# Performance work log

Measured on AMD Instinct MI355X. Metric: run time of the kernel, lower is better.

Reference implementation:

```python
import jax, jax.numpy as jnp
import numpy as np

B, N, K = 8, 4096, 5


def setup_inputs() -> dict:
    key = jax.random.key(0)
    ks = jax.random.split(key, 24)
    s = 0.05
    inp = {
        'pointcloud': jax.random.normal(ks[0], (B, 3, N, 1), jnp.float32),
        # local 1x1 conv stack (bias-free) + BN affine params (eval mode, stats=identity)
        'conv_w1': jax.random.normal(ks[1], (64, 3), jnp.float32) * s,
        'bn1_g': jnp.ones((64,), jnp.float32), 'bn1_b': jnp.zeros((64,), jnp.float32),
        'conv_w2': jax.random.normal(ks[2], (64, 64), jnp.float32) * s,
        'bn2_g': jnp.ones((64,), jnp.float32), 'bn2_b': jnp.zeros((64,), jnp.float32),
        'conv_w3': jax.random.normal(ks[3], (64, 64), jnp.float32) * s,
        'bn3_g': jnp.ones((64,), jnp.float32), 'bn3_b': jnp.zeros((64,), jnp.float32),
        'conv_w4': jax.random.normal(ks[4], (128, 64), jnp.float32) * s,
        'bn4_g': jnp.ones((128,), jnp.float32), 'bn4_b': jnp.zeros((128,), jnp.float32),
        # GCN layers
        'gc1_w': jax.random.normal(ks[5], (128, 128), jnp.float32) * s,
        'gc1_b': jnp.zeros((128,), jnp.float32),
        'gc2_w': jax.random.normal(ks[6], (128, 128), jnp.float32) * s,
        'gc2_b': jnp.zeros((128,), jnp.float32),
        'gc3_w': jax.random.normal(ks[7], (128, 256), jnp.float32) * s,
        'gc3_b': jnp.zeros((256,), jnp.float32),
        # MLP head
        'fc1_w': jax.random.normal(ks[8], (512, 256), jnp.float32) * s,
        'bnf1_g': jnp.ones((512,), jnp.float32), 'bnf1_b': jnp.zeros((512,), jnp.float32),
        'fc2_w': jax.random.normal(ks[9], (256, 512), jnp.float32) * s,
        'bnf2_g': jnp.ones((256,), jnp.float32), 'bnf2_b': jnp.zeros((256,), jnp.float32),
        'fc3_w': jax.random.normal(ks[10], (128, 256), jnp.float32) * s,
        'fc3_b': jnp.zeros((128,), jnp.float32),
    }
    return inp


def _cbr(h, w, g, b):
    # 1x1 conv (per-point linear) + BatchNorm(eval, identity stats) + ReLU
    return jax.nn.relu((h @ w.T) * g + b)


def reference(pointcloud, conv_w1, bn1_g, bn1_b, conv_w2, bn2_g, bn2_b,
              conv_w3, bn3_g, bn3_b, conv_w4, bn4_g, bn4_b,
              gc1_w, gc1_b, gc2_w, gc2_b, gc3_w, gc3_b,
              fc1_w, bnf1_g, bnf1_b, fc2_w, bnf2_g, bnf2_b, fc3_w, fc3_b):
    pts = pointcloud[..., 0]                       # [B,3,N]
    b, _, n = pts.shape

    # ---- LocalOperation: sort points by distance to centroid, gather ----
    centroid = pts.mean(axis=2, keepdims=True)     # [B,3,1]
    d_cent = ((pts - centroid) ** 2).sum(axis=1)   # [B,N]
    order = jnp.argsort(d_cent, axis=-1)           # [B,N]
    x = jnp.take_along_axis(pts, order[:, None, :], axis=2)  # [B,3,N]

    h = x.transpose(0, 2, 1)                       # [B,N,3]
    h = _cbr(h, conv_w1, bn1_g, bn1_b)             # [B,N,64]
    h = _cbr(h, conv_w2, bn2_g, bn2_b)
    h = _cbr(h, conv_w3, bn3_g, bn3_b)
    h = _cbr(h, conv_w4, bn4_g, bn4_b)             # [B,N,128]
    feat = h.reshape(b * n, 128)                   # node features

    # ---- KNN graph (k=5, within each cloud, self included like KDTree) ----
    sq = (pts ** 2).sum(axis=1)                                        # [B,N]
    d2 = sq[:, :, None] + sq[:, None, :] - 2.0 * jnp.einsum('bcn,bcm->bnm', pts, pts)
    _, nbr = jax.lax.top_k(-d2, K)                                     # [B,N,K]
    offsets = (jnp.arange(b) * n)[:, None, None]
    src = (nbr + offsets).reshape(-1)                                  # [B*N*K]
    dst = jnp.broadcast_to(jnp.arange(b * n).reshape(b, n, 1), (b, n, K)).reshape(-1)

    num_nodes = b * n
    ones = jnp.ones_like(src, jnp.float32)
    deg_out = jax.ops.segment_sum(ones, src, num_segments=num_nodes)
    deg_in = jax.ops.segment_sum(ones, dst, num_segments=num_nodes)
    norm_out = jax.lax.rsqrt(jnp.maximum(deg_out, 1.0))
    norm_in = jax.lax.rsqrt(jnp.maximum(deg_in, 1.0))

    def gcn(hh, w, bias):
        hw = (hh @ w) * norm_out[:, None]          # [BN,F] pre-normed features
        msg = hw[src]                              # gather
        agg = jax.ops.segment_sum(msg, dst, num_segments=num_nodes)  # scatter-add
        return agg * norm_in[:, None] + bias

    g = jax.nn.relu(gcn(feat, gc1_w, gc1_b))       # [BN,128]
    g = jax.nn.relu(gcn(g, gc2_w, gc2_b))          # [BN,128]
    g = gcn(g, gc3_w, gc3_b)                       # [BN,256]

    # ---- head (BN eval, dropout eval = identity) ----
    z = jax.nn.relu((g @ fc1_w.T) * bnf1_g + bnf1_b)   # [BN,512]
    z = jax.nn.relu((z @ fc2_w.T) * bnf2_g + bnf2_b)   # [BN,256]
    pooled = z.max(axis=0)                             # [256] global max over nodes
    out = pooled @ fc3_w.T + fc3_b                     # [128]
    return out
```

## Files before the change

kernel.cpp:

```cpp
#include <hip/hip_runtime.h>
#include <math.h>
#include <float.h>

#define NB 8
#define NP 4096
#define BN_ (NB*NP)
#define KNN 5
#define JCH 512
#define NJC (NP/JCH)

typedef unsigned short u16;
typedef __attribute__((ext_vector_type(8))) __bf16 bf16x8;
typedef __attribute__((ext_vector_type(4))) float f32x4;

__device__ __forceinline__ u16 f2bf(float x){
  unsigned u = __float_as_uint(x);
  u += 0x7fff + ((u>>16)&1);
  return (u16)(u>>16);
}
__device__ __forceinline__ float bf2f(u16 h){ return __uint_as_float(((unsigned)h)<<16); }


__global__ void k_centroid(const float* __restrict__ pc, float* __restrict__ dcent) {
  int b = blockIdx.x, tid = threadIdx.x;
  const float* px = pc + (size_t)b*3*NP;
  const float* py = px + NP;
  const float* pz = py + NP;
  double sx=0, sy=0, sz=0;
  for (int n = tid; n < NP; n += 256) { sx += px[n]; sy += py[n]; sz += pz[n]; }
  __shared__ double rx[256], ry[256], rz[256];
  rx[tid]=sx; ry[tid]=sy; rz[tid]=sz;
  __syncthreads();
  for (int s = 128; s > 0; s >>= 1) {
    if (tid < s) { rx[tid]+=rx[tid+s]; ry[tid]+=ry[tid+s]; rz[tid]+=rz[tid+s]; }
    __syncthreads();
  }
  __shared__ float cxs, cys, czs;
  if (tid == 0) {
    cxs = (float)(rx[0]/NP); cys = (float)(ry[0]/NP); czs = (float)(rz[0]/NP);
  }
  __syncthreads();
  float cx = cxs, cy = cys, cz = czs;
  for (int n = tid; n < NP; n += 256) {
    float dx = __fsub_rn(px[n], cx);
    float dy = __fsub_rn(py[n], cy);
    float dz = __fsub_rn(pz[n], cz);
    float d = __fadd_rn(__fadd_rn(__fmul_rn(dx,dx), __fmul_rn(dy,dy)), __fmul_rn(dz,dz));
    dcent[b*NP + n] = d;
  }
}

__global__ void __launch_bounds__(256) k_rank_part(const float* __restrict__ dcent,
                                                   int* __restrict__ rank) {
  int jc = blockIdx.x, ic = blockIdx.y, b = blockIdx.z;
  __shared__ float d[JCH];
  int j0 = jc*JCH;
  for (int n = threadIdx.x; n < JCH; n += 256) d[n] = dcent[b*NP + j0 + n];
  __syncthreads();
  int i = ic*256 + threadIdx.x;
  float di = dcent[b*NP + i];
  int cnt = 0;
  #pragma unroll 8
  for (int n = 0; n < JCH; ++n) {
    float dj = d[n];
    cnt += (dj < di) || (dj == di && (j0 + n) < i);
  }
  atomicAdd(&rank[b*NP + i], cnt);
}

__global__ void k_scatter(const int* __restrict__ rank, int* __restrict__ ord) {
  int idx = blockIdx.x*256 + threadIdx.x;
  int b = idx >> 12, i = idx & (NP-1);
  ord[b*NP + rank[idx]] = i;
}

__global__ void k_prep(const float* __restrict__ pc, const int* __restrict__ ord,
                       const float* __restrict__ dcent,
                       float4* __restrict__ srt, float* __restrict__ rc) {
  int idx = blockIdx.x*256 + threadIdx.x;
  int b = idx >> 12;
  int oi = ord[idx];
  const float* base = pc + (size_t)b*3*NP;
  float x = base[oi], y = base[NP+oi], z = base[2*NP+oi];
  float sq = __fadd_rn(__fadd_rn(__fmul_rn(x,x), __fmul_rn(y,y)), __fmul_rn(z,z));
  float4 v; v.x=x; v.y=y; v.z=z; v.w=sq;
  srt[idx] = v;
  rc[idx] = sqrtf(dcent[b*NP + oi]);
}

#define INS(dist, q) \
  if (dist < b4) { \
    if (dist < b3) { b4=b3; r4=r3; \
      if (dist < b2) { b3=b2; r3=r2; \
        if (dist < b1) { b2=b1; r2=r1; \
          if (dist < b0) { b1=b0; r1=r0; b0=dist; r0=(q); } \
          else { b1=dist; r1=(q); } \
        } else { b2=dist; r2=(q); } \
      } else { b3=dist; r3=(q); } \
    } else { b4=dist; r4=(q); } \
  }

__global__ void __launch_bounds__(256) k_knn_ann3(const float4* __restrict__ srt,
                                                  const float* __restrict__ rc,
                                                  const int* __restrict__ ord,
                                                  int* __restrict__ nbr,
                                                  int* __restrict__ deg) {
  __shared__ float4 tile[NP];
  __shared__ float rtile[NP];
  int b = blockIdx.x >> 7;
  int blk = blockIdx.x & 127;
  int gbase = b*NP;
  for (int t = threadIdx.x; t < NP; t += 256) {
    tile[t] = srt[gbase + t];
    rtile[t] = rc[gbase + t];
  }
  __syncthreads();

  const int lane = threadIdx.x & 63;
  const int wv   = threadIdx.x >> 6;
  const int grp  = lane >> 3;
  const int sub  = lane & 7;
  const int s_i  = blk*32 + wv*8 + grp;

  float4 p = tile[s_i];
  float xi=p.x, yi=p.y, zi=p.z, sqi=p.w;
  float ri = rtile[s_i];

  const bool is_hi = (sub < 4);
  int j = is_hi ? (s_i + sub) : (s_i - 1 - (sub - 4));
  const int step = is_hi ? 4 : -4;

  float b0=FLT_MAX, b1=FLT_MAX, b2=FLT_MAX, b3=FLT_MAX, b4=FLT_MAX;
  int r0=0, r1=0, r2=0, r3=0, r4=0;
  bool alive = ((unsigned)j < NP);

  while (__ballot(alive)) {
    int q[8]; float4 jp[8];
    #pragma unroll
    for (int t = 0; t < 8; ++t) {
      int qq = j + step*t;
      int qc = qq < 0 ? 0 : (qq > NP-1 ? NP-1 : qq);
      q[t] = qq;
      jp[t] = tile[qc];
    }
    #pragma unroll
    for (int t = 0; t < 8; ++t) {
      float dot = __fadd_rn(__fadd_rn(__fmul_rn(xi,jp[t].x), __fmul_rn(yi,jp[t].y)), __fmul_rn(zi,jp[t].z));
      float dist = __fsub_rn(__fadd_rn(sqi, jp[t].w), __fmul_rn(2.0f, dot));
      bool valid = alive && ((unsigned)q[t] < NP);
      if (!valid) dist = FLT_MAX;
      if (dist < b4) { INS(dist, q[t]) }
    }
    float bm = b4;
    bm = fminf(bm, __shfl_xor(bm, 1));
    bm = fminf(bm, __shfl_xor(bm, 2));
    bm = fminf(bm, __shfl_xor(bm, 4));
    float T = bm*1.0002f + 1e-9f;
    int qe = j + step*7;
    int qec = qe < 0 ? 0 : (qe > NP-1 ? NP-1 : qe);
    float dr = fabsf(ri - rtile[qec]);
    j += step*8;
    alive = alive && ((unsigned)j < NP) && (__fmul_rn(dr,dr) < T);
  }

  #pragma unroll
  for (int m = 1; m <= 4; m <<= 1) {
    float c0=__shfl_xor(b0,m), c1=__shfl_xor(b1,m), c2=__shfl_xor(b2,m),
          c3=__shfl_xor(b3,m), c4=__shfl_xor(b4,m);
    int   s0=__shfl_xor(r0,m), s1=__shfl_xor(r1,m), s2=__shfl_xor(r2,m),
          s3=__shfl_xor(r3,m), s4=__shfl_xor(r4,m);
    if (c0 < b4) { INS(c0, s0)
      if (c1 < b4) { INS(c1, s1)
        if (c2 < b4) { INS(c2, s2)
          if (c3 < b4) { INS(c3, s3)
            if (c4 < b4) { INS(c4, s4) }
          }
        }
      }
    }
  }

  if (sub == 0) {
    int oi = ord[gbase + s_i];
    int node = gbase + oi;
    int nb = node*KNN;
    int o0 = gbase + ord[gbase+r0], o1 = gbase + ord[gbase+r1], o2 = gbase + ord[gbase+r2];
    int o3 = gbase + ord[gbase+r3], o4 = gbase + ord[gbase+r4];
    nbr[nb+0]=o0; nbr[nb+1]=o1; nbr[nb+2]=o2; nbr[nb+3]=o3; nbr[nb+4]=o4;
    atomicAdd(&deg[o0],1); atomicAdd(&deg[o1],1); atomicAdd(&deg[o2],1);
    atomicAdd(&deg[o3],1); atomicAdd(&deg[o4],1);
  }
}

__global__ void k_norm(const int* __restrict__ deg, float* __restrict__ normo) {
  int i = blockIdx.x*256 + threadIdx.x;
  int d = deg[i]; if (d < 1) d = 1;
  normo[i] = 1.0f / sqrtf((float)d);
}

__global__ void k_cvt_all(const float* __restrict__ w2, const float* __restrict__ w3,
                          const float* __restrict__ w4, const float* __restrict__ gc1,
                          const float* __restrict__ gc2, const float* __restrict__ gc3,
                          const float* __restrict__ fc1, const float* __restrict__ fc2,
                          u16* o2, u16* o3, u16* o4, u16* og1, u16* og2, u16* og3,
                          u16* of1, u16* of2) {
  int i = blockIdx.x*256 + threadIdx.x;
  if (i < 4096) { o2[i] = f2bf(w2[i]); return; } i -= 4096;
  if (i < 4096) { o3[i] = f2bf(w3[i]); return; } i -= 4096;
  if (i < 8192) { o4[i] = f2bf(w4[i]); return; } i -= 8192;
  if (i < 16384) { int n=i>>7, k=i&127; og1[i] = f2bf(gc1[k*128+n]); return; } i -= 16384;
  if (i < 16384) { int n=i>>7, k=i&127; og2[i] = f2bf(gc2[k*128+n]); return; } i -= 16384;
  if (i < 32768) { int n=i>>7, k=i&127; og3[i] = f2bf(gc3[k*256+n]); return; } i -= 32768;
  if (i < 131072) { of1[i] = f2bf(fc1[i]); return; } i -= 131072;
  if (i < 131072) { of2[i] = f2bf(fc2[i]); }
}

__global__ void k_conv1(const float* __restrict__ pc, const int* __restrict__ ord,
                        const float* __restrict__ w, const float* __restrict__ g,
                        const float* __restrict__ bias, u16* __restrict__ outp) {
  int node = blockIdx.x*4 + (threadIdx.x >> 6);
  int o = threadIdx.x & 63;
  int b = node >> 12;
  int j = ord[node];
  const float* base = pc + (size_t)b*3*NP;
  float x = base[j], y = base[NP + j], z = base[2*NP + j];
  float acc = x*w[o*3+0] + y*w[o*3+1] + z*w[o*3+2];
  float v = fmaxf(acc*g[o] + bias[o], 0.0f);
  outp[(size_t)node*64 + o] = f2bf(v);
}

template<int BNT>
__global__ __launch_bounds__(256) void gemm_bf16(
    const u16* __restrict__ A, const u16* __restrict__ W,
    const float* __restrict__ gamma, const float* __restrict__ beta,
    const float* __restrict__ rowscale, void* __restrict__ Cout,
    int K, int Nc, int mode) {
  constexpr int NF = BNT/32;
  __shared__ u16 As[128*64];
  __shared__ u16 Bs[BNT*64];
  const int tid = threadIdx.x;
  const int w = tid >> 6, l = tid & 63;
  const int m0 = blockIdx.x*128, n0 = blockIdx.y*BNT;
  const int wm = w & 1, wn = w >> 1;
  const int lr = l >> 3;
  const int lc = l & 7;
  const int fm = l & 15, fk = l >> 4;

  f32x4 acc[4][NF];
  #pragma unroll
  for (int i=0;i<4;++i)
    #pragma unroll
    for (int j=0;j<NF;++j) acc[i][j] = (f32x4){0.f,0.f,0.f,0.f};

  for (int k0 = 0; k0 < K; k0 += 64) {
    #pragma unroll
    for (int t=0;t<4;++t){
      int row = (w*4 + t)*8 + lr;
      uint4 v = *(const uint4*)(A + ((size_t)(m0+row)*K + k0 + lc*8));
      *(uint4*)&As[row*64 + ((lc ^ (row&7))*8)] = v;
    }
    #pragma unroll
    for (int t=0;t<NF;++t){
      int row = (w*NF + t)*8 + lr;
      uint4 v = *(const uint4*)(W + ((size_t)(n0+row)*K + k0 + lc*8));
      *(uint4*)&Bs[row*64 + ((lc ^ (row&7))*8)] = v;
    }
    __syncthreads();
    #pragma unroll
    for (int ks=0; ks<2; ++ks){
      bf16x8 af[4], bfr[NF];
      #pragma unroll
      for (int mf=0; mf<4; ++mf){
        int row = wm*64 + mf*16 + fm;
        int ck = ks*4 + fk;
        af[mf] = *(const bf16x8*)&As[row*64 + ((ck ^ (row&7))*8)];
      }
      #pragma unroll
      for (int nf=0; nf<NF; ++nf){
        int row = wn*(BNT/2) + nf*16 + fm;
        int ck = ks*4 + fk;
        bfr[nf] = *(const bf16x8*)&Bs[row*64 + ((ck ^ (row&7))*8)];
      }
      #pragma unroll
      for (int mf=0; mf<4; ++mf)
        #pragma unroll
        for (int nf=0; nf<NF; ++nf)
          acc[mf][nf] = __builtin_amdgcn_mfma_f32_16x16x32_bf16(af[mf], bfr[nf], acc[mf][nf], 0, 0, 0);
    }
    __syncthreads();
  }

  const int col_base = n0 + wn*(BNT/2);
  if (mode == 1) {
    u16* C = (u16*)Cout;
    #pragma unroll
    for (int mf=0; mf<4; ++mf){
      #pragma unroll
      for (int r=0;r<4;++r){
        int row = m0 + wm*64 + mf*16 + fk*4 + r;
        float rs = rowscale[row];
        #pragma unroll
        for (int nf=0;nf<NF;++nf){
          int col = col_base + nf*16 + fm;
          C[(size_t)row*Nc + col] = f2bf(acc[mf][nf][r]*rs);
        }
      }
    }
  } else {
    float gv[NF], bv[NF];
    #pragma unroll
    for (int nf=0;nf<NF;++nf){
      int col = col_base + nf*16 + fm;
      gv[nf] = gamma[col]; bv[nf] = beta[col];
    }
    #pragma unroll
    for (int mf=0; mf<4; ++mf){
      #pragma unroll
      for (int r=0;r<4;++r){
        int row = m0 + wm*64 + mf*16 + fk*4 + r;
        #pragma unroll
        for (int nf=0;nf<NF;++nf){
          int col = col_base + nf*16 + fm;
          float v = fmaxf(acc[mf][nf][r]*gv[nf] + bv[nf], 0.f);
          if (mode == 0) ((u16*)Cout)[(size_t)row*Nc + col] = f2bf(v);
          else           ((float*)Cout)[(size_t)row*Nc + col] = v;
        }
      }
    }
  }
}

__global__ void k_agg_bf(const u16* __restrict__ hw, const int* __restrict__ nbr,
                         const float* __restrict__ bias, u16* __restrict__ outp,
                         int F, int do_relu) {
  int per = F >> 3;
  int gid = blockIdx.x*256 + threadIdx.x;
  int i = gid / per;
  int f = (gid - i*per) * 8;
  const int* nb = nbr + i*KNN;
  float s[8] = {0,0,0,0,0,0,0,0};
  #pragma unroll
  for (int k = 0; k < KNN; ++k) {
    uint4 v = *(const uint4*)(hw + (size_t)nb[k]*F + f);
    const u16* h = (const u16*)&v;
    #pragma unroll
    for (int j=0;j<8;++j) s[j] += bf2f(h[j]);
  }
  const float ninv = 0.44721359549995793f;
  u16 o[8];
  #pragma unroll
  for (int j=0;j<8;++j){
    float v = s[j]*ninv + bias[f+j];
    if (do_relu) v = fmaxf(v, 0.f);
    o[j] = f2bf(v);
  }
  *(uint4*)&outp[(size_t)i*F + f] = *(const uint4*)o;
}

__global__ void k_maxpool(const float* __restrict__ z, unsigned int* __restrict__ pooled) {
  int o = threadIdx.x;
  int r0 = blockIdx.x * 128;
  float m = 0.0f;
  for (int r = 0; r < 128; ++r) m = fmaxf(m, z[(size_t)(r0 + r)*256 + o]);
  atomicMax(&pooled[o], __float_as_uint(m));
}

__global__ void k_fc3(const float* __restrict__ pooled, const float* __restrict__ w,
                      const float* __restrict__ bias, float* __restrict__ outp) {
  __shared__ float p[256];
  int tid = threadIdx.x;
  p[tid] = pooled[tid];
  p[tid + 128] = pooled[tid + 128];
  __syncthreads();
  float s = 0.0f;
  for (int i = 0; i < 256; ++i) s = fmaf(w[tid*256 + i], p[i], s);
  outp[tid] = s + bias[tid];
}

extern "C" void kernel_launch(void* const* d_in, const int* in_sizes, int n_in,
                              void* d_out, int out_size, void* d_ws, size_t ws_size,
                              hipStream_t stream) {
  const float* pc   = (const float*)d_in[0];
  const float* w1   = (const float*)d_in[1];
  const float* g1   = (const float*)d_in[2];
  const float* b1   = (const float*)d_in[3];
  const float* w2   = (const float*)d_in[4];
  const float* g2   = (const float*)d_in[5];
  const float* b2   = (const float*)d_in[6];
  const float* w3   = (const float*)d_in[7];
  const float* g3   = (const float*)d_in[8];
  const float* b3   = (const float*)d_in[9];
  const float* w4   = (const float*)d_in[10];
  const float* g4   = (const float*)d_in[11];
  const float* b4   = (const float*)d_in[12];
  const float* gc1w = (const float*)d_in[13];
  const float* gc1b = (const float*)d_in[14];
  const float* gc2w = (const float*)d_in[15];
  const float* gc2b = (const float*)d_in[16];
  const float* gc3w = (const float*)d_in[17];
  const float* gc3b = (const float*)d_in[18];
  const float* fc1w = (const float*)d_in[19];
  const float* f1g  = (const float*)d_in[20];
  const float* f1b  = (const float*)d_in[21];
  const float* fc2w = (const float*)d_in[22];
  const float* f2g  = (const float*)d_in[23];
  const float* f2b  = (const float*)d_in[24];
  const float* fc3w = (const float*)d_in[25];
  const float* fc3b = (const float*)d_in[26];
  float* outp = (float*)d_out;

  char* wsb = (char*)d_ws;
  size_t off = 0;
  auto alloc = [&](size_t bytes) -> void* {
    void* p = wsb + off;
    off += (bytes + 255) & ~(size_t)255;
    return p;
  };
  int*   ord    = (int*)  alloc((size_t)BN_*4);
  int*   deg    = (int*)  alloc((size_t)BN_*4);
  int*   rankb  = (int*)  alloc((size_t)BN_*4);
  int*   nbr    = (int*)  alloc((size_t)BN_*KNN*4);
  float* dcent  = (float*)alloc((size_t)BN_*4);
  float* normo  = (float*)alloc((size_t)BN_*4);
  float* pooled = (float*)alloc(256*4);
  float4* srt   = (float4*)alloc((size_t)BN_*16);
  float* rc     = (float*)alloc((size_t)BN_*4);
  u16* wb2   = (u16*)alloc(64*64*2);
  u16* wb3   = (u16*)alloc(64*64*2);
  u16* wb4   = (u16*)alloc(128*64*2);
  u16* wgc1  = (u16*)alloc(128*128*2);
  u16* wgc2  = (u16*)alloc(128*128*2);
  u16* wgc3  = (u16*)alloc(256*128*2);
  u16* wfc1  = (u16*)alloc(512*256*2);
  u16* wfc2  = (u16*)alloc(256*512*2);
  u16* h1   = (u16*)alloc((size_t)BN_*64*2);
  u16* h2   = (u16*)alloc((size_t)BN_*64*2);
  u16* feat = (u16*)alloc((size_t)BN_*128*2);
  u16* hw   = (u16*)alloc((size_t)BN_*256*2);
  u16* gb1  = (u16*)alloc((size_t)BN_*128*2);
  u16* g3b  = (u16*)alloc((size_t)BN_*256*2);
  u16* z1   = (u16*)alloc((size_t)BN_*512*2);
  float* z2 = (float*)alloc((size_t)BN_*256*4);

  hipMemsetAsync(deg, 0, (size_t)BN_*4, stream);
  hipMemsetAsync(rankb, 0, (size_t)BN_*4, stream);
  hipMemsetAsync(pooled, 0, 256*4, stream);

  k_cvt_all<<<1344, 256, 0, stream>>>(w2, w3, w4, gc1w, gc2w, gc3w, fc1w, fc2w,
                                      wb2, wb3, wb4, wgc1, wgc2, wgc3, wfc1, wfc2);

  k_centroid<<<NB, 256, 0, stream>>>(pc, dcent);
  k_rank_part<<<dim3(NJC, NP/256, NB), 256, 0, stream>>>(dcent, rankb);
  k_scatter<<<BN_/256, 256, 0, stream>>>(rankb, ord);
  k_prep<<<BN_/256, 256, 0, stream>>>(pc, ord, dcent, srt, rc);
  k_knn_ann3<<<NB*128, 256, 0, stream>>>(srt, rc, ord, nbr, deg);
  k_norm<<<BN_/256, 256, 0, stream>>>(deg, normo);

  k_conv1<<<BN_/4, 256, 0, stream>>>(pc, ord, w1, g1, b1, h1);
  gemm_bf16<64><<<dim3(BN_/128, 1), 256, 0, stream>>>(h1, wb2, g2, b2, nullptr, h2, 64, 64, 0);
  gemm_bf16<64><<<dim3(BN_/128, 1), 256, 0, stream>>>(h2, wb3, g3, b3, nullptr, h1, 64, 64, 0);
  gemm_bf16<128><<<dim3(BN_/128, 1), 256, 0, stream>>>(h1, wb4, g4, b4, nullptr, feat, 64, 128, 0);

  gemm_bf16<128><<<dim3(BN_/128, 1), 256, 0, stream>>>(feat, wgc1, nullptr, nullptr, normo, hw, 128, 128, 1);
  k_agg_bf<<<(BN_*16)/256, 256, 0, stream>>>(hw, nbr, gc1b, gb1, 128, 1);
  gemm_bf16<128><<<dim3(BN_/128, 1), 256, 0, stream>>>(gb1, wgc2, nullptr, nullptr, normo, hw, 128, 128, 1);
  k_agg_bf<<<(BN_*16)/256, 256, 0, stream>>>(hw, nbr, gc2b, feat, 128, 1);
  gemm_bf16<128><<<dim3(BN_/128, 2), 256, 0, stream>>>(feat, wgc3, nullptr, nullptr, normo, hw, 128, 256, 1);
  k_agg_bf<<<(BN_*32)/256, 256, 0, stream>>>(hw, nbr, gc3b, g3b, 256, 0);

  gemm_bf16<128><<<dim3(BN_/128, 4), 256, 0, stream>>>(g3b, wfc1, f1g, f1b, nullptr, z1, 256, 512, 0);
  gemm_bf16<128><<<dim3(BN_/128, 2), 256, 0, stream>>>(z1, wfc2, f2g, f2b, nullptr, z2, 512, 256, 2);
  k_maxpool<<<BN_/128, 256, 0, stream>>>(z2, (unsigned int*)pooled);
  k_fc3<<<1, 128, 0, stream>>>(pooled, fc3w, fc3b, outp);
}
```

Baseline: 411.8 us.

## Fuse scatter/prep, drop memsets and norm kernel, sentinel-padded 512-thread KNN

Merges the rank scatter and point prep into one kernel that writes sorted data directly. The three memsets are replaced by zeroing inside existing kernels, and the separate norm kernel is removed by computing rsqrt(degree) in the GEMM epilogue. The KNN kernel gets 512-thread blocks and a sentinel-padded shared tile, which removes per-candidate clamping and validity checks, plus a wave-uniform ballot guard on insertion. The aim is fewer launches and less per-iteration work in the KNN search. The trade-off is higher shared-memory and register demand per block and recomputing the norm on every GEMM.

```diff
diff --git a/kernel.cpp b/kernel.cpp
--- a/kernel.cpp
+++ b/kernel.cpp
@@ -8,6 +8,7 @@
 #define KNN 5
 #define JCH 512
 #define NJC (NP/JCH)
+#define SENT 64
 
 typedef unsigned short u16;
 typedef __attribute__((ext_vector_type(8))) __bf16 bf16x8;
@@ -21,7 +22,8 @@
 __device__ __forceinline__ float bf2f(u16 h){ return __uint_as_float(((unsigned)h)<<16); }
 
 
-__global__ void k_centroid(const float* __restrict__ pc, float* __restrict__ dcent) {
+__global__ void k_centroid(const float* __restrict__ pc, float* __restrict__ dcent,
+                           int* __restrict__ rankb) {
   int b = blockIdx.x, tid = threadIdx.x;
   const float* px = pc + (size_t)b*3*NP;
   const float* py = px + NP;
@@ -47,6 +49,7 @@
     float dz = __fsub_rn(pz[n], cz);
     float d = __fadd_rn(__fadd_rn(__fmul_rn(dx,dx), __fmul_rn(dy,dy)), __fmul_rn(dz,dz));
     dcent[b*NP + n] = d;
+    rankb[b*NP + n] = 0;
   }
 }
 
@@ -68,24 +71,21 @@
   atomicAdd(&rank[b*NP + i], cnt);
 }
 
-__global__ void k_scatter(const int* __restrict__ rank, int* __restrict__ ord) {
+__global__ void k_scatprep(const float* __restrict__ pc, const int* __restrict__ rank,
+                           const float* __restrict__ dcent,
+                           int* __restrict__ ord, float4* __restrict__ srt,
+                           float* __restrict__ rcv, int* __restrict__ deg) {
   int idx = blockIdx.x*256 + threadIdx.x;
   int b = idx >> 12, i = idx & (NP-1);
-  ord[b*NP + rank[idx]] = i;
-}
-
-__global__ void k_prep(const float* __restrict__ pc, const int* __restrict__ ord,
-                       const float* __restrict__ dcent,
-                       float4* __restrict__ srt, float* __restrict__ rc) {
-  int idx = blockIdx.x*256 + threadIdx.x;
-  int b = idx >> 12;
-  int oi = ord[idx];
+  int r = rank[idx];
+  ord[b*NP + r] = i;
   const float* base = pc + (size_t)b*3*NP;
-  float x = base[oi], y = base[NP+oi], z = base[2*NP+oi];
+  float x = base[i], y = base[NP+i], z = base[2*NP+i];
   float sq = __fadd_rn(__fadd_rn(__fmul_rn(x,x), __fmul_rn(y,y)), __fmul_rn(z,z));
   float4 v; v.x=x; v.y=y; v.z=z; v.w=sq;
-  srt[idx] = v;
-  rc[idx] = sqrtf(dcent[b*NP + oi]);
+  srt[b*NP + r] = v;
+  rcv[b*NP + r] = sqrtf(dcent[idx]);
+  deg[idx] = 0;
 }
 
 #define INS(dist, q) \
@@ -100,19 +100,20 @@
     } else { b4=dist; r4=(q); } \
   }
 
-__global__ void __launch_bounds__(256) k_knn_ann3(const float4* __restrict__ srt,
+__global__ void __launch_bounds__(512) k_knn_ann4(const float4* __restrict__ srt,
                                                   const float* __restrict__ rc,
                                                   const int* __restrict__ ord,
                                                   int* __restrict__ nbr,
                                                   int* __restrict__ deg) {
-  __shared__ float4 tile[NP];
-  __shared__ float rtile[NP];
-  int b = blockIdx.x >> 7;
-  int blk = blockIdx.x & 127;
+  __shared__ float4 tile[NP + 2*SENT];
+  __shared__ float rtile[NP + 2*SENT];
+  int b = blockIdx.x >> 6;
+  int blk = blockIdx.x & 63;
   int gbase = b*NP;
-  for (int t = threadIdx.x; t < NP; t += 256) {
-    tile[t] = srt[gbase + t];
-    rtile[t] = rc[gbase + t];
+  for (int t = threadIdx.x; t < NP + 2*SENT; t += 512) {
+    int q = t - SENT;
+    if ((unsigned)q < NP) { tile[t] = srt[gbase + q]; rtile[t] = rc[gbase + q]; }
+    else { float4 s4; s4.x=0.f; s4.y=0.f; s4.z=0.f; s4.w=1e30f; tile[t] = s4; rtile[t] = 0.f; }
   }
   __syncthreads();
 
@@ -120,47 +121,41 @@
   const int wv   = threadIdx.x >> 6;
   const int grp  = lane >> 3;
   const int sub  = lane & 7;
-  const int s_i  = blk*32 + wv*8 + grp;
-
-  float4 p = tile[s_i];
+  const int s_i  = blk*64 + wv*8 + grp;
+
+  float4 p = tile[SENT + s_i];
   float xi=p.x, yi=p.y, zi=p.z, sqi=p.w;
-  float ri = rtile[s_i];
+  float ri = rtile[SENT + s_i];
 
   const bool is_hi = (sub < 4);
+  const int step = is_hi ? 4 : -4;
+  const int jdead = is_hi ? (NP + 7) : (-36);
   int j = is_hi ? (s_i + sub) : (s_i - 1 - (sub - 4));
-  const int step = is_hi ? 4 : -4;
+  bool alive = ((unsigned)j < NP);
+  if (!alive) j = jdead;
 
   float b0=FLT_MAX, b1=FLT_MAX, b2=FLT_MAX, b3=FLT_MAX, b4=FLT_MAX;
   int r0=0, r1=0, r2=0, r3=0, r4=0;
-  bool alive = ((unsigned)j < NP);
 
   while (__ballot(alive)) {
-    int q[8]; float4 jp[8];
-    #pragma unroll
-    for (int t = 0; t < 8; ++t) {
-      int qq = j + step*t;
-      int qc = qq < 0 ? 0 : (qq > NP-1 ? NP-1 : qq);
-      q[t] = qq;
-      jp[t] = tile[qc];
-    }
+    float4 jp[8];
+    #pragma unroll
+    for (int t = 0; t < 8; ++t) jp[t] = tile[SENT + j + step*t];
     #pragma unroll
     for (int t = 0; t < 8; ++t) {
       float dot = __fadd_rn(__fadd_rn(__fmul_rn(xi,jp[t].x), __fmul_rn(yi,jp[t].y)), __fmul_rn(zi,jp[t].z));
       float dist = __fsub_rn(__fadd_rn(sqi, jp[t].w), __fmul_rn(2.0f, dot));
-      bool valid = alive && ((unsigned)q[t] < NP);
-      if (!valid) dist = FLT_MAX;
-      if (dist < b4) { INS(dist, q[t]) }
+      if (__ballot(dist < b4)) { INS(dist, j + step*t) }
     }
     float bm = b4;
     bm = fminf(bm, __shfl_xor(bm, 1));
     bm = fminf(bm, __shfl_xor(bm, 2));
     bm = fminf(bm, __shfl_xor(bm, 4));
     float T = bm*1.0002f + 1e-9f;
-    int qe = j + step*7;
-    int qec = qe < 0 ? 0 : (qe > NP-1 ? NP-1 : qe);
-    float dr = fabsf(ri - rtile[qec]);
-    j += step*8;
-    alive = alive && ((unsigned)j < NP) && (__fmul_rn(dr,dr) < T);
+    float dr = fabsf(ri - rtile[SENT + j + step*7]);
+    bool nextin = ((unsigned)(j + step*8) < NP);
+    alive = alive && nextin && (__fmul_rn(dr,dr) < T);
+    j = alive ? (j + step*8) : jdead;
   }
 
   #pragma unroll
@@ -190,12 +185,6 @@
     atomicAdd(&deg[o0],1); atomicAdd(&deg[o1],1); atomicAdd(&deg[o2],1);
     atomicAdd(&deg[o3],1); atomicAdd(&deg[o4],1);
   }
-}
-
-__global__ void k_norm(const int* __restrict__ deg, float* __restrict__ normo) {
-  int i = blockIdx.x*256 + threadIdx.x;
-  int d = deg[i]; if (d < 1) d = 1;
-  normo[i] = 1.0f / sqrtf((float)d);
 }
 
 __global__ void k_cvt_all(const float* __restrict__ w2, const float* __restrict__ w3,
@@ -217,7 +206,9 @@
 
 __global__ void k_conv1(const float* __restrict__ pc, const int* __restrict__ ord,
                         const float* __restrict__ w, const float* __restrict__ g,
-                        const float* __restrict__ bias, u16* __restrict__ outp) {
+                        const float* __restrict__ bias, u16* __restrict__ outp,
+                        float* __restrict__ pooled) {
+  if (blockIdx.x == 0) pooled[threadIdx.x] = 0.0f;
   int node = blockIdx.x*4 + (threadIdx.x >> 6);
   int o = threadIdx.x & 63;
   int b = node >> 12;
@@ -233,7 +224,7 @@
 __global__ __launch_bounds__(256) void gemm_bf16(
     const u16* __restrict__ A, const u16* __restrict__ W,
     const float* __restrict__ gamma, const float* __restrict__ beta,
-    const float* __restrict__ rowscale, void* __restrict__ Cout,
+    const int* __restrict__ degp, void* __restrict__ Cout,
     int K, int Nc, int mode) {
   constexpr int NF = BNT/32;
   __shared__ u16 As[128*64];
@@ -298,7 +289,8 @@
       #pragma unroll
       for (int r=0;r<4;++r){
         int row = m0 + wm*64 + mf*16 + fk*4 + r;
-        float rs = rowscale[row];
+        int d = degp[row]; if (d < 1) d = 1;
+        float rs = 1.0f / sqrtf((float)d);
         #pragma unroll
         for (int nf=0;nf<NF;++nf){
           int col = col_base + nf*16 + fm;
@@ -421,7 +413,6 @@
   int*   rankb  = (int*)  alloc((size_t)BN_*4);
   int*   nbr    = (int*)  alloc((size_t)BN_*KNN*4);
   float* dcent  = (float*)alloc((size_t)BN_*4);
-  float* normo  = (float*)alloc((size_t)BN_*4);
   float* pooled = (float*)alloc(256*4);
   float4* srt   = (float4*)alloc((size_t)BN_*16);
   float* rc     = (float*)alloc((size_t)BN_*4);
@@ -442,30 +433,24 @@
   u16* z1   = (u16*)alloc((size_t)BN_*512*2);
   float* z2 = (float*)alloc((size_t)BN_*256*4);
 
-  hipMemsetAsync(deg, 0, (size_t)BN_*4, stream);
-  hipMemsetAsync(rankb, 0, (size_t)BN_*4, stream);
-  hipMemsetAsync(pooled, 0, 256*4, stream);
-
   k_cvt_all<<<1344, 256, 0, stream>>>(w2, w3, w4, gc1w, gc2w, gc3w, fc1w, fc2w,
                                       wb2, wb3, wb4, wgc1, wgc2, wgc3, wfc1, wfc2);
 
-  k_centroid<<<NB, 256, 0, stream>>>(pc, dcent);
+  k_centroid<<<NB, 256, 0, stream>>>(pc, dcent, rankb);
   k_rank_part<<<dim3(NJC, NP/256, NB), 256, 0, stream>>>(dcent, rankb);
-  k_scatter<<<BN_/256, 256, 0, stream>>>(rankb, ord);
-  k_prep<<<BN_/256, 256, 0, stream>>>(pc, ord, dcent, srt, rc);
-  k_knn_ann3<<<NB*128, 256, 0, stream>>>(srt, rc, ord, nbr, deg);
-  k_norm<<<BN_/256, 256, 0, stream>>>(deg, normo);
-
-  k_conv1<<<BN_/4, 256, 0, stream>>>(pc, ord, w1, g1, b1, h1);
+  k_scatprep<<<BN_/256, 256, 0, stream>>>(pc, rankb, dcent, ord, srt, rc, deg);
+  k_knn_ann4<<<NB*64, 512, 0, stream>>>(srt, rc, ord, nbr, deg);
+
+  k_conv1<<<BN_/4, 256, 0, stream>>>(pc, ord, w1, g1, b1, h1, pooled);
   gemm_bf16<64><<<dim3(BN_/128, 1), 256, 0, stream>>>(h1, wb2, g2, b2, nullptr, h2, 64, 64, 0);
   gemm_bf16<64><<<dim3(BN_/128, 1), 256, 0, stream>>>(h2, wb3, g3, b3, nullptr, h1, 64, 64, 0);
   gemm_bf16<128><<<dim3(BN_/128, 1), 256, 0, stream>>>(h1, wb4, g4, b4, nullptr, feat, 64, 128, 0);
 
-  gemm_bf16<128><<<dim3(BN_/128, 1), 256, 0, stream>>>(feat, wgc1, nullptr, nullptr, normo, hw, 128, 128, 1);
+  gemm_bf16<128><<<dim3(BN_/128, 1), 256, 0, stream>>>(feat, wgc1, nullptr, nullptr, deg, hw, 128, 128, 1);
   k_agg_bf<<<(BN_*16)/256, 256, 0, stream>>>(hw, nbr, gc1b, gb1, 128, 1);
-  gemm_bf16<128><<<dim3(BN_/128, 1), 256, 0, stream>>>(gb1, wgc2, nullptr, nullptr, normo, hw, 128, 128, 1);
+  gemm_bf16<128><<<dim3(BN_/128, 1), 256, 0, stream>>>(gb1, wgc2, nullptr, nullptr, deg, hw, 128, 128, 1);
   k_agg_bf<<<(BN_*16)/256, 256, 0, stream>>>(hw, nbr, gc2b, feat, 128, 1);
-  gemm_bf16<128><<<dim3(BN_/128, 2), 256, 0, stream>>>(feat, wgc3, nullptr, nullptr, normo, hw, 128, 256, 1);
+  gemm_bf16<128><<<dim3(BN_/128, 2), 256, 0, stream>>>(feat, wgc3, nullptr, nullptr, deg, hw, 128, 256, 1);
   k_agg_bf<<<(BN_*32)/256, 256, 0, stream>>>(hw, nbr, gc3b, g3b, 256, 0);
 
   gemm_bf16<128><<<dim3(BN_/128, 4), 256, 0, stream>>>(g3b, wfc1, f1g, f1b, nullptr, z1, 256, 512, 0);
```

Measured after the change: 405.3 us. Within noise of the previous version (-1.6%).
